# Optimization experiments

Measured on AMD Instinct MI355X. Metric: run time of the kernel, lower is better.

Reference implementation:

```python
import jax, jax.numpy as jnp
import numpy as np
import math

BS, L, DIM, H = 2, 1024, 1024, 16
DPH = DIM // H            # 64 dim per head
PHI_DIM = DPH * 1         # phi_size_ratio = 1
N_PROJS = 200
MIN_LOG_STD = math.log(1e-5)
SQRT_PHI = math.sqrt(PHI_DIM)


def setup_inputs() -> dict:
    key = jax.random.key(0)
    ks = jax.random.split(key, 8)
    lin = lambda k: jax.random.normal(k, (DIM, DIM), jnp.float32) * 0.02
    return {
        "x": jax.random.normal(ks[0], (BS, L, DIM), jnp.float32),
        "mask": jnp.ones((BS, L), dtype=jnp.bool_),
        "Wq": lin(ks[1]), "bq": jnp.zeros((DIM,), jnp.float32),
        "Wk": lin(ks[2]), "bk": jnp.zeros((DIM,), jnp.float32),
        "Wv": lin(ks[3]), "bv": jnp.zeros((DIM,), jnp.float32),
        "Wo": lin(ks[4]), "bo": jnp.zeros((DIM,), jnp.float32),
        "log_sigma": jnp.zeros((H, 1, DPH), jnp.float32),  # log(1.0) init
        "random_projs": jax.random.normal(ks[5], (N_PROJS, PHI_DIM, DPH), jnp.float32),
    }


def _phi(x, rp_scaled):
    # x: (b, l, h, d); rp_scaled: (h, phi, d). arccos features: relu(proj) / sqrt(phi_dim)
    x = x / jnp.maximum(jnp.linalg.norm(x, axis=-1, keepdims=True), 1e-12)
    px = jnp.einsum('blhd,hpd->blhp', x, rp_scaled)
    return jax.nn.relu(px) / SQRT_PHI


def _causal_rfa(phi_q, phi_k, v):
    # sequential S,z recurrence, time-major scan
    def step(carry, inp):
        S, z = carry
        pk, pq, vt = inp                       # (b,h,phi),(b,h,phi),(b,h,d)
        S = S + pk[..., :, None] * vt[..., None, :]
        z = z + pk
        num = jnp.einsum('bhp,bhpd->bhd', pq, S)
        den = jnp.einsum('bhp,bhp->bh', pq, z)
        return (S, z), num / jnp.maximum(den, 1e-5)[..., None]

    S0 = jnp.zeros((BS, H, PHI_DIM, DPH), jnp.float32)
    z0 = jnp.zeros((BS, H, PHI_DIM), jnp.float32)
    xs = (jnp.transpose(phi_k, (1, 0, 2, 3)),
          jnp.transpose(phi_q, (1, 0, 2, 3)),
          jnp.transpose(v, (1, 0, 2, 3)))
    _, h_t = jax.lax.scan(step, (S0, z0), xs)  # (l, b, h, d)
    return jnp.transpose(h_t, (1, 0, 2, 3))     # (b, l, h, d)


def reference(x, mask, Wq, bq, Wk, bk, Wv, bv, Wo, bo, log_sigma, random_projs):
    q = (x @ Wq.T + bq).reshape(BS, L, H, DPH)
    k = (x @ Wk.T + bk).reshape(BS, L, H, DPH)
    v = (x @ Wv.T + bv).reshape(BS, L, H, DPH)
    # eval mode: proj_id = 0 for every head
    scale = jnp.exp(jnp.maximum(log_sigma, MIN_LOG_STD))                  # (h,1,d)
    rp = scale * jnp.broadcast_to(random_projs[0], (H, PHI_DIM, DPH))     # (h,phi,d)
    phi_q = _phi(q, rp)
    phi_k = _phi(k, rp) * mask[:, :, None, None].astype(jnp.float32)
    h = _causal_rfa(phi_q, phi_k, v)                                      # (b,l,h,d)
    return h.reshape(BS, L, DIM) @ Wo.T + bo
```

## Files before the change

kernel.cpp:

```cpp
#include <hip/hip_runtime.h>


typedef unsigned short ushort_t;
typedef __attribute__((ext_vector_type(8))) __bf16 bf16x8;
typedef __attribute__((ext_vector_type(4))) float f32x4;

#define MLS -11.512925464970229f

__device__ __forceinline__ ushort_t f2b(float f) {
  union { float f; unsigned u; } v; v.f = f;
  unsigned r = v.u + 0x7FFFu + ((v.u >> 16) & 1u);
  return (ushort_t)(r >> 16);
}

__device__ __forceinline__ void gload16(const void* g, void* l) {
  __builtin_amdgcn_global_load_lds((__attribute__((address_space(1))) void*)(void*)g,
                                   (__attribute__((address_space(3))) void*)l, 16, 0, 0);
}

__device__ __forceinline__ f32x4 mfma_bf16(bf16x8 a, bf16x8 b, f32x4 c) {
  return __builtin_amdgcn_mfma_f32_16x16x32_bf16(a, b, c, 0, 0, 0);
}

__global__ __launch_bounds__(256) void convert_kernel(
    const float* __restrict__ x, const float* __restrict__ Wq, const float* __restrict__ Wk,
    const float* __restrict__ Wv, const float* __restrict__ Wo,
    const float* __restrict__ bq, const float* __restrict__ bk, const float* __restrict__ bv,
    const float* __restrict__ lsig, const float* __restrict__ rp0,
    ushort_t* __restrict__ xb, ushort_t* __restrict__ Wcat, ushort_t* __restrict__ Wob,
    float* __restrict__ bcat, float* __restrict__ sclbuf, ushort_t* __restrict__ rpb) {
  const size_t NX = (size_t)1 << 21, NW = (size_t)1 << 20;
  const size_t nch = (NX + 4 * NW) >> 3;
  size_t stride = (size_t)gridDim.x * 256;
  for (size_t i = (size_t)blockIdx.x * 256 + threadIdx.x; i < nch + 1024; i += stride) {
    if (i < nch) {
      size_t e = i << 3;
      const float* src; ushort_t* dst;
      if (e < NX)            { src = x  + e;               dst = xb   + e; }
      else if (e < NX + NW)  { src = Wq + (e - NX);        dst = Wcat + (e - NX); }
      else if (e < NX + 2*NW){ src = Wk + (e - NX - NW);   dst = Wcat + (e - NX); }
      else if (e < NX + 3*NW){ src = Wv + (e - NX - 2*NW); dst = Wcat + (e - NX); }
      else                   { src = Wo + (e - NX - 3*NW); dst = Wob  + (e - NX - 3*NW); }
      float4 a = *(const float4*)src, c = *(const float4*)(src + 4);
      uint4 u;
      u.x = (unsigned)f2b(a.x) | ((unsigned)f2b(a.y) << 16);
      u.y = (unsigned)f2b(a.z) | ((unsigned)f2b(a.w) << 16);
      u.z = (unsigned)f2b(c.x) | ((unsigned)f2b(c.y) << 16);
      u.w = (unsigned)f2b(c.z) | ((unsigned)f2b(c.w) << 16);
      *(uint4*)dst = u;
    } else {
      int j = (int)(i - nch);
      sclbuf[j] = expf(fmaxf(lsig[j], MLS));
      bcat[j] = bq[j]; bcat[1024 + j] = bk[j]; bcat[2048 + j] = bv[j];
#pragma unroll
      for (int jj = 0; jj < 4; ++jj) {
        int pe = j * 4 + jj;
        rpb[pe] = f2b(rp0[pe]);
      }
    }
  }
}

__global__ __launch_bounds__(256, 3) void qkvphi_kernel(
    const ushort_t* __restrict__ A, const ushort_t* __restrict__ Bm,
    const float* __restrict__ bias, const float* __restrict__ sclbuf,
    const ushort_t* __restrict__ rpb,
    ushort_t* __restrict__ phiq, ushort_t* __restrict__ phik, ushort_t* __restrict__ vbT) {
  __shared__ __align__(16) ushort_t smem[24576];
  const int K = 1024;
  int blk = blockIdx.x;
  int bx = blk % 48, by = blk / 48;
  int m0 = by << 7, n0 = bx << 6;
  int region = bx >> 4;
  int tid = threadIdx.x;
  int w = tid >> 6, l = tid & 63;
  int wm = w << 5;
  int lr = l & 15, lg = l >> 4;
  bf16x8 rpf[2][4];
  if (region < 2) {
#pragma unroll
    for (int kk = 0; kk < 2; ++kk)
#pragma unroll
      for (int ni = 0; ni < 4; ++ni)
        rpf[kk][ni] = *(const bf16x8*)(rpb + (ni*16 + lr)*64 + kk*32 + lg*8);
  }
  f32x4 acc[2][4] = {};
  auto stage = [&](int buf, int k0) {
    ushort_t* Ad = smem + buf*8192;
    ushort_t* Bd = smem + 16384 + buf*4096;
#pragma unroll
    for (int it = 0; it < 4; ++it) {
      int idx = it*256 + tid, row = idx >> 3, cg = idx & 7;
      gload16(A + (size_t)(m0 + row)*K + k0 + ((cg ^ (row & 7)) << 3), Ad + idx*8);
    }
#pragma unroll
    for (int it = 0; it < 2; ++it) {
      int idx = it*256 + tid, row = idx >> 3, cg = idx & 7;
      gload16(Bm + (size_t)(n0 + row)*K + k0 + ((cg ^ (row & 7)) << 3), Bd + idx*8);
    }
  };
  auto compute = [&](int buf) {
    const ushort_t* Ab = smem + buf*8192;
    const ushort_t* Bb = smem + 16384 + buf*4096;
#pragma unroll
    for (int kk = 0; kk < 2; ++kk) {
      bf16x8 af[2], bfr[4];
#pragma unroll
      for (int i = 0; i < 2; ++i) {
        int r = wm + i*16 + lr;
        af[i] = *(const bf16x8*)(Ab + r*64 + (((kk*4 + lg) ^ (r & 7)) << 3));
      }
#pragma unroll
      for (int i = 0; i < 4; ++i) {
        int r = i*16 + lr;
        bfr[i] = *(const bf16x8*)(Bb + r*64 + (((kk*4 + lg) ^ (r & 7)) << 3));
      }
#pragma unroll
      for (int mi = 0; mi < 2; ++mi)
#pragma unroll
        for (int ni = 0; ni < 4; ++ni)
          acc[mi][ni] = mfma_bf16(af[mi], bfr[ni], acc[mi][ni]);
    }
  };
  stage(0, 0);
  for (int t = 0; t < 15; ++t) {
    stage((t + 1) & 1, (t + 1) * 64);
    asm volatile("s_waitcnt vmcnt(6)" ::: "memory");
    __builtin_amdgcn_s_barrier();
    compute(t & 1);
    asm volatile("s_waitcnt lgkmcnt(0)" ::: "memory");
    __builtin_amdgcn_s_barrier();
  }
  asm volatile("s_waitcnt vmcnt(0)" ::: "memory");
  __builtin_amdgcn_s_barrier();
  compute(1);

  int b = m0 >> 10, tloc0 = m0 & 1023;
  float bias4[4];
#pragma unroll
  for (int ni = 0; ni < 4; ++ni) bias4[ni] = bias[n0 + ni*16 + lr];
  if (region == 2) {
    int dbase = n0 & 1023;
    int h = dbase >> 6;
    size_t hbase = ((size_t)(b*16 + h) << 16);
#pragma unroll
    for (int mi = 0; mi < 2; ++mi)
#pragma unroll
      for (int ni = 0; ni < 4; ++ni) {
        int d = (dbase + ni*16 + lr) & 63;
#pragma unroll
        for (int r = 0; r < 4; ++r) {
          int t = tloc0 + wm + mi*16 + lg*4 + r;
          int lloc = t & 127;
          int sv = (lloc & 7) | ((((lloc >> 3) ^ (d & 15)) & 15) << 3);
          vbT[hbase + (size_t)d*1024 + (t >> 7)*128 + sv] = f2b(acc[mi][ni][r] + bias4[ni]);
        }
      }
  } else {
    ushort_t* Ys = smem;
    int hglob = bx & 15;
    float scl4[4];
#pragma unroll
    for (int ni = 0; ni < 4; ++ni) scl4[ni] = sclbuf[hglob*64 + ni*16 + lr];
#pragma unroll
    for (int mi = 0; mi < 2; ++mi) {
      float v4[4][4];
      float ss[4] = {0.f, 0.f, 0.f, 0.f};
#pragma unroll
      for (int ni = 0; ni < 4; ++ni)
#pragma unroll
        for (int r = 0; r < 4; ++r) {
          float vv = acc[mi][ni][r] + bias4[ni];
          v4[ni][r] = vv;
          ss[r] += vv * vv;
        }
#pragma unroll
      for (int r = 0; r < 4; ++r) {
        float s = ss[r];
        s += __shfl_xor(s, 1); s += __shfl_xor(s, 2);
        s += __shfl_xor(s, 4); s += __shfl_xor(s, 8);
        ss[r] = 1.f / fmaxf(sqrtf(s), 1e-12f);
      }
#pragma unroll
      for (int ni = 0; ni < 4; ++ni) {
        int c = ni*16 + lr;
#pragma unroll
        for (int r = 0; r < 4; ++r) {
          int rl = wm + mi*16 + lg*4 + r;
          Ys[rl*64 + (((c >> 3) ^ (rl & 7)) << 3) + (c & 7)] = f2b(v4[ni][r] * ss[r] * scl4[ni]);
        }
      }
    }
    __syncthreads();
    ushort_t* dst = region ? phik : phiq;
    size_t obase = ((size_t)(b*16 + hglob) << 16);
    f32x4 acc2[2][4] = {};
#pragma unroll
    for (int kk = 0; kk < 2; ++kk) {
      bf16x8 af2[2];
#pragma unroll
      for (int mi = 0; mi < 2; ++mi) {
        int r = wm + mi*16 + lr;
        af2[mi] = *(const bf16x8*)(Ys + r*64 + (((kk*4 + lg) ^ (r & 7)) << 3));
      }
#pragma unroll
      for (int mi = 0; mi < 2; ++mi)
#pragma unroll
        for (int ni = 0; ni < 4; ++ni)
          acc2[mi][ni] = mfma_bf16(af2[mi], rpf[kk][ni], acc2[mi][ni]);
    }
#pragma unroll
    for (int mi = 0; mi < 2; ++mi)
#pragma unroll
      for (int ni = 0; ni < 4; ++ni)
#pragma unroll
        for (int r = 0; r < 4; ++r) {
          int t = tloc0 + wm + mi*16 + lg*4 + r;
          int p = ni*16 + lr;
          float val = fmaxf(acc2[mi][ni][r], 0.f) * 0.125f;
          int sp = (p & 7) | ((((p >> 3) ^ (t & 7)) & 7) << 3);
          dst[obase + (size_t)t*64 + sp] = f2b(val);
        }
  }
}

__global__ __launch_bounds__(256) void outproj_kernel(
    const ushort_t* __restrict__ A, const ushort_t* __restrict__ Bm,
    const float* __restrict__ bias, float* __restrict__ C) {
  __shared__ __align__(16) ushort_t smem[16384];
  const int K = 1024;
  int wid = (blockIdx.x & 7) * 64 + (blockIdx.x >> 3);
  int bx = wid & 15, by = wid >> 4;
  int m0 = by << 6, n0 = bx << 6;
  int tid = threadIdx.x, w = tid >> 6, l = tid & 63;
  int lr = l & 15, lg = l >> 4;
  auto stage = [&](int buf, int k0) {
    ushort_t* Ad = smem + buf*4096;
    ushort_t* Bd = smem + 8192 + buf*4096;
#pragma unroll
    for (int it = 0; it < 2; ++it) {
      int idx = it*256 + tid, row = idx >> 3, cg = idx & 7;
      gload16(A + (size_t)(m0 + row)*K + k0 + ((cg ^ (row & 7)) << 3), Ad + idx*8);
    }
#pragma unroll
    for (int it = 0; it < 2; ++it) {
      int idx = it*256 + tid, row = idx >> 3, cg = idx & 7;
      gload16(Bm + (size_t)(n0 + row)*K + k0 + ((cg ^ (row & 7)) << 3), Bd + idx*8);
    }
  };
  f32x4 acc[4] = {};
  auto compute = [&](int buf) {
    const ushort_t* Ab = smem + buf*4096;
    const ushort_t* Bb = smem + 8192 + buf*4096;
#pragma unroll
    for (int kk = 0; kk < 2; ++kk) {
      int ra = w*16 + lr;
      bf16x8 af = *(const bf16x8*)(Ab + ra*64 + (((kk*4 + lg) ^ (ra & 7)) << 3));
      bf16x8 bfr[4];
#pragma unroll
      for (int i = 0; i < 4; ++i) {
        int rb = i*16 + lr;
        bfr[i] = *(const bf16x8*)(Bb + rb*64 + (((kk*4 + lg) ^ (rb & 7)) << 3));
      }
#pragma unroll
      for (int ni = 0; ni < 4; ++ni)
        acc[ni] = mfma_bf16(af, bfr[ni], acc[ni]);
    }
  };
  stage(0, 0);
  for (int t = 0; t < 15; ++t) {
    stage((t + 1) & 1, (t + 1) * 64);
    asm volatile("s_waitcnt vmcnt(4)" ::: "memory");
    __builtin_amdgcn_s_barrier();
    compute(t & 1);
    asm volatile("s_waitcnt lgkmcnt(0)" ::: "memory");
    __builtin_amdgcn_s_barrier();
  }
  asm volatile("s_waitcnt vmcnt(0)" ::: "memory");
  __builtin_amdgcn_s_barrier();
  compute(1);
#pragma unroll
  for (int ni = 0; ni < 4; ++ni) {
    int col = n0 + ni*16 + lr;
    float bv = bias[col];
#pragma unroll
    for (int r = 0; r < 4; ++r)
      C[(size_t)(m0 + w*16 + lg*4 + r)*1024 + col] = acc[ni][r] + bv;
  }
}

__global__ __launch_bounds__(256) void attn_kernel(
    const ushort_t* __restrict__ phiq, const ushort_t* __restrict__ phik,
    const ushort_t* __restrict__ vbT, ushort_t* __restrict__ hb) {
  __shared__ __align__(16) ushort_t Qs[8192];
  __shared__ __align__(16) ushort_t Kd[2*8192];
  __shared__ __align__(16) ushort_t Vd[2*8192];
  __shared__ __align__(16) ushort_t Ps[16384];
  __shared__ float den_lds[128];
  int blk = blockIdx.x;
  int qt = blk >> 5, bh = blk & 31;
  int b = bh >> 4, h = bh & 15;
  int tid = threadIdx.x, w = tid >> 6, l = tid & 63;
  int lr = l & 15, lg = l >> 4;
  const ushort_t* pq = phiq + ((size_t)bh << 16) + qt*8192;
  const ushort_t* pk = phik + ((size_t)bh << 16);
  const ushort_t* pv = vbT  + ((size_t)bh << 16);
#pragma unroll
  for (int it = 0; it < 4; ++it) {
    int idx = it*256 + tid;
    gload16(pq + idx*8, Qs + idx*8);
  }
  auto stageKV = [&](int buf, int kt) {
#pragma unroll
    for (int it = 0; it < 4; ++it) {
      int idx = it*256 + tid;
      gload16(pk + kt*8192 + idx*8, Kd + buf*8192 + idx*8);
      gload16(pv + (idx >> 4)*1024 + kt*128 + (idx & 15)*8, Vd + buf*8192 + idx*8);
    }
  };
  f32x4 nacc[2][4] = {};
  float den[2] = {0.f, 0.f};
  auto tile = [&](int buf, bool diag) {
    const ushort_t* Ks = Kd + buf*8192;
    const ushort_t* Vs = Vd + buf*8192;
    bf16x8 qf[2][2];
#pragma unroll
    for (int qi = 0; qi < 2; ++qi)
#pragma unroll
      for (int ks = 0; ks < 2; ++ks) {
        int q = w*32 + qi*16 + lr;
        qf[qi][ks] = *(const bf16x8*)(Qs + q*64 + (((ks*4 + lg) ^ (q & 7)) << 3));
      }
    f32x4 sfr[8][2] = {};
#pragma unroll
    for (int kf = 0; kf < 8; ++kf) {
#pragma unroll
      for (int ks = 0; ks < 2; ++ks) {
        int kloc = kf*16 + lr;
        bf16x8 af = *(const bf16x8*)(Ks + kloc*64 + (((ks*4 + lg) ^ (kloc & 7)) << 3));
        sfr[kf][0] = mfma_bf16(af, qf[0][ks], sfr[kf][0]);
        sfr[kf][1] = mfma_bf16(af, qf[1][ks], sfr[kf][1]);
      }
    }
#pragma unroll
    for (int kf = 0; kf < 8; ++kf) {
#pragma unroll
      for (int qi = 0; qi < 2; ++qi) {
        int q = w*32 + qi*16 + lr;
        f32x4 v4 = sfr[kf][qi];
        if (diag) {
          int keyb = kf*16 + lg*4;
#pragma unroll
          for (int r = 0; r < 4; ++r)
            if (keyb + r > q) v4[r] = 0.f;
        }
        den[qi] += v4[0] + v4[1] + v4[2] + v4[3];
        unsigned long long u = (unsigned long long)f2b(v4[0])
                             | ((unsigned long long)f2b(v4[1]) << 16)
                             | ((unsigned long long)f2b(v4[2]) << 32)
                             | ((unsigned long long)f2b(v4[3]) << 48);
        int chunk = (2*kf + (lg >> 1)) ^ (q & 7);
        *(unsigned long long*)(Ps + q*128 + chunk*8 + (lg & 1)*4) = u;
      }
    }
#pragma unroll
    for (int ks = 0; ks < 4; ++ks) {
      bf16x8 pa[2];
#pragma unroll
      for (int qi = 0; qi < 2; ++qi) {
        int q = w*32 + qi*16 + lr;
        pa[qi] = *(const bf16x8*)(Ps + q*128 + (((4*ks + lg) ^ (q & 7)) << 3));
      }
#pragma unroll
      for (int df = 0; df < 4; ++df) {
        int d = df*16 + lr;
        bf16x8 vf = *(const bf16x8*)(Vs + d*128 + (((4*ks + lg) ^ (d & 15)) << 3));
        nacc[0][df] = mfma_bf16(pa[0], vf, nacc[0][df]);
        nacc[1][df] = mfma_bf16(pa[1], vf, nacc[1][df]);
      }
    }
  };
  stageKV(0, 0);
  for (int kt = 0; kt < qt; ++kt) {
    stageKV((kt + 1) & 1, kt + 1);
    asm volatile("s_waitcnt vmcnt(8)" ::: "memory");
    __builtin_amdgcn_s_barrier();
    tile(kt & 1, false);
    asm volatile("s_waitcnt lgkmcnt(0)" ::: "memory");
    __builtin_amdgcn_s_barrier();
  }
  asm volatile("s_waitcnt vmcnt(0)" ::: "memory");
  __builtin_amdgcn_s_barrier();
  tile(qt & 1, true);
  den[0] += __shfl_xor(den[0], 16); den[0] += __shfl_xor(den[0], 32);
  den[1] += __shfl_xor(den[1], 16); den[1] += __shfl_xor(den[1], 32);
  if (lg == 0) {
    den_lds[w*32 + lr]      = den[0];
    den_lds[w*32 + 16 + lr] = den[1];
  }
  __syncthreads();
#pragma unroll
  for (int qi = 0; qi < 2; ++qi)
#pragma unroll
    for (int df = 0; df < 4; ++df)
#pragma unroll
      for (int r = 0; r < 4; ++r) {
        int qloc = w*32 + qi*16 + lg*4 + r;
        int d = df*16 + lr;
        float dd = fmaxf(den_lds[qloc], 1e-5f);
        float val = nacc[qi][df][r] / dd;
        hb[((size_t)(b*1024 + qt*128 + qloc))*1024 + h*64 + d] = f2b(val);
      }
}

extern "C" void kernel_launch(void* const* d_in, const int* in_sizes, int n_in,
                              void* d_out, int out_size, void* d_ws, size_t ws_size,
                              hipStream_t stream) {
  const float* x  = (const float*)d_in[0];
  const float* Wq = (const float*)d_in[2];
  const float* bq = (const float*)d_in[3];
  const float* Wk = (const float*)d_in[4];
  const float* bk = (const float*)d_in[5];
  const float* Wv = (const float*)d_in[6];
  const float* bv = (const float*)d_in[7];
  const float* Wo = (const float*)d_in[8];
  const float* bo = (const float*)d_in[9];
  const float* ls = (const float*)d_in[10];
  const float* rp = (const float*)d_in[11];

  char* ws = (char*)d_ws;
  size_t off = 0;
  auto alloc = [&](size_t bytes) { char* p = ws + off; off += (bytes + 255) & ~(size_t)255; return p; };
  ushort_t* xb     = (ushort_t*)alloc((size_t)2048*1024*2);
  ushort_t* Wcat   = (ushort_t*)alloc((size_t)3072*1024*2);
  ushort_t* Wob    = (ushort_t*)alloc((size_t)1024*1024*2);
  float*    bcat   = (float*)   alloc((size_t)3072*4);
  float*    sclbuf = (float*)   alloc((size_t)1024*4);
  ushort_t* rpb    = (ushort_t*)alloc((size_t)64*64*2);
  ushort_t* phiq   = (ushort_t*)alloc((size_t)32*1024*64*2);
  ushort_t* phik   = (ushort_t*)alloc((size_t)32*1024*64*2);
  ushort_t* vbT    = (ushort_t*)alloc((size_t)32*64*1024*2);
  ushort_t* hb     = (ushort_t*)alloc((size_t)2048*1024*2);

  convert_kernel<<<1024, 256, 0, stream>>>(x, Wq, Wk, Wv, Wo, bq, bk, bv, ls, rp,
                                           xb, Wcat, Wob, bcat, sclbuf, rpb);
  qkvphi_kernel<<<768, 256, 0, stream>>>(xb, Wcat, bcat, sclbuf, rpb, phiq, phik, vbT);
  attn_kernel<<<256, 256, 0, stream>>>(phiq, phik, vbT, hb);
  outproj_kernel<<<512, 256, 0, stream>>>(hb, Wob, bo, (float*)d_out);
}
```

Baseline: 62.17 us.

## Compute Q, K and V for one head per block with 512-thread tiles

Restructures the QKV+phi GEMM so each block covers a 128-row tile across all of Q, K and V for a single head (192 output columns), using 8 waves instead of 4. Waves split into Q/K halves that each also take half of the V columns, and each wave normalizes and projects its own 32x64 slice through a private LDS region. The A tile is now loaded once for all three projections, which cuts redundant x traffic. In exchange the grid shrinks from 768 blocks to 256, and each block uses more LDS and registers, which may lower occupancy on a GPU with many CUs.

```diff
diff --git a/kernel.cpp b/kernel.cpp
--- a/kernel.cpp
+++ b/kernel.cpp
@@ -61,71 +61,70 @@
   }
 }
 
-__global__ __launch_bounds__(256, 3) void qkvphi_kernel(
+__global__ __launch_bounds__(512, 2) void qkvphi_kernel(
     const ushort_t* __restrict__ A, const ushort_t* __restrict__ Bm,
     const float* __restrict__ bias, const float* __restrict__ sclbuf,
     const ushort_t* __restrict__ rpb,
     ushort_t* __restrict__ phiq, ushort_t* __restrict__ phik, ushort_t* __restrict__ vbT) {
-  __shared__ __align__(16) ushort_t smem[24576];
+  __shared__ __align__(16) ushort_t smem[40960];
   const int K = 1024;
   int blk = blockIdx.x;
-  int bx = blk % 48, by = blk / 48;
-  int m0 = by << 7, n0 = bx << 6;
-  int region = bx >> 4;
+  int hg = blk & 15, by = blk >> 4;
+  int m0 = by << 7;
   int tid = threadIdx.x;
   int w = tid >> 6, l = tid & 63;
-  int wm = w << 5;
+  int wr = w & 3, wc = w >> 2;
   int lr = l & 15, lg = l >> 4;
   bf16x8 rpf[2][4];
-  if (region < 2) {
-#pragma unroll
-    for (int kk = 0; kk < 2; ++kk)
-#pragma unroll
-      for (int ni = 0; ni < 4; ++ni)
-        rpf[kk][ni] = *(const bf16x8*)(rpb + (ni*16 + lr)*64 + kk*32 + lg*8);
-  }
-  f32x4 acc[2][4] = {};
+#pragma unroll
+  for (int kk = 0; kk < 2; ++kk)
+#pragma unroll
+    for (int ni = 0; ni < 4; ++ni)
+      rpf[kk][ni] = *(const bf16x8*)(rpb + (ni*16 + lr)*64 + kk*32 + lg*8);
+
+  f32x4 acc[2][6] = {};
   auto stage = [&](int buf, int k0) {
     ushort_t* Ad = smem + buf*8192;
-    ushort_t* Bd = smem + 16384 + buf*4096;
-#pragma unroll
-    for (int it = 0; it < 4; ++it) {
-      int idx = it*256 + tid, row = idx >> 3, cg = idx & 7;
+    ushort_t* Bd = smem + 16384 + buf*12288;
+#pragma unroll
+    for (int it = 0; it < 2; ++it) {
+      int idx = it*512 + tid, row = idx >> 3, cg = idx & 7;
       gload16(A + (size_t)(m0 + row)*K + k0 + ((cg ^ (row & 7)) << 3), Ad + idx*8);
     }
 #pragma unroll
-    for (int it = 0; it < 2; ++it) {
-      int idx = it*256 + tid, row = idx >> 3, cg = idx & 7;
-      gload16(Bm + (size_t)(n0 + row)*K + k0 + ((cg ^ (row & 7)) << 3), Bd + idx*8);
+    for (int it = 0; it < 3; ++it) {
+      int idx = it*512 + tid, row = idx >> 3, cg = idx & 7;
+      int grow = (row >> 6)*1024 + hg*64 + (row & 63);
+      gload16(Bm + (size_t)grow*K + k0 + ((cg ^ (row & 7)) << 3), Bd + idx*8);
     }
   };
   auto compute = [&](int buf) {
     const ushort_t* Ab = smem + buf*8192;
-    const ushort_t* Bb = smem + 16384 + buf*4096;
+    const ushort_t* Bb = smem + 16384 + buf*12288;
 #pragma unroll
     for (int kk = 0; kk < 2; ++kk) {
-      bf16x8 af[2], bfr[4];
+      bf16x8 af[2], bfr[6];
 #pragma unroll
       for (int i = 0; i < 2; ++i) {
-        int r = wm + i*16 + lr;
+        int r = wr*32 + i*16 + lr;
         af[i] = *(const bf16x8*)(Ab + r*64 + (((kk*4 + lg) ^ (r & 7)) << 3));
       }
 #pragma unroll
-      for (int i = 0; i < 4; ++i) {
-        int r = i*16 + lr;
-        bfr[i] = *(const bf16x8*)(Bb + r*64 + (((kk*4 + lg) ^ (r & 7)) << 3));
+      for (int i = 0; i < 6; ++i) {
+        int brow = (i < 4) ? (wc*64 + i*16 + lr) : (128 + wc*32 + (i - 4)*16 + lr);
+        bfr[i] = *(const bf16x8*)(Bb + brow*64 + (((kk*4 + lg) ^ (brow & 7)) << 3));
       }
 #pragma unroll
       for (int mi = 0; mi < 2; ++mi)
 #pragma unroll
-        for (int ni = 0; ni < 4; ++ni)
+        for (int ni = 0; ni < 6; ++ni)
           acc[mi][ni] = mfma_bf16(af[mi], bfr[ni], acc[mi][ni]);
     }
   };
   stage(0, 0);
   for (int t = 0; t < 15; ++t) {
     stage((t + 1) & 1, (t + 1) * 64);
-    asm volatile("s_waitcnt vmcnt(6)" ::: "memory");
+    asm volatile("s_waitcnt vmcnt(5)" ::: "memory");
     __builtin_amdgcn_s_barrier();
     compute(t & 1);
     asm volatile("s_waitcnt lgkmcnt(0)" ::: "memory");
@@ -134,34 +133,36 @@
   asm volatile("s_waitcnt vmcnt(0)" ::: "memory");
   __builtin_amdgcn_s_barrier();
   compute(1);
+  __syncthreads();
 
   int b = m0 >> 10, tloc0 = m0 & 1023;
-  float bias4[4];
-#pragma unroll
-  for (int ni = 0; ni < 4; ++ni) bias4[ni] = bias[n0 + ni*16 + lr];
-  if (region == 2) {
-    int dbase = n0 & 1023;
-    int h = dbase >> 6;
-    size_t hbase = ((size_t)(b*16 + h) << 16);
+  {
+    size_t hbase = ((size_t)(b*16 + hg) << 16);
+    float bv2[2];
+#pragma unroll
+    for (int j = 0; j < 2; ++j) bv2[j] = bias[2048 + hg*64 + wc*32 + j*16 + lr];
 #pragma unroll
     for (int mi = 0; mi < 2; ++mi)
 #pragma unroll
-      for (int ni = 0; ni < 4; ++ni) {
-        int d = (dbase + ni*16 + lr) & 63;
+      for (int j = 0; j < 2; ++j) {
+        int d = wc*32 + j*16 + lr;
 #pragma unroll
         for (int r = 0; r < 4; ++r) {
-          int t = tloc0 + wm + mi*16 + lg*4 + r;
+          int t = tloc0 + wr*32 + mi*16 + lg*4 + r;
           int lloc = t & 127;
           int sv = (lloc & 7) | ((((lloc >> 3) ^ (d & 15)) & 15) << 3);
-          vbT[hbase + (size_t)d*1024 + (t >> 7)*128 + sv] = f2b(acc[mi][ni][r] + bias4[ni]);
+          vbT[hbase + (size_t)d*1024 + (t >> 7)*128 + sv] = f2b(acc[mi][4 + j][r] + bv2[j]);
         }
       }
-  } else {
-    ushort_t* Ys = smem;
-    int hglob = bx & 15;
-    float scl4[4];
-#pragma unroll
-    for (int ni = 0; ni < 4; ++ni) scl4[ni] = sclbuf[hglob*64 + ni*16 + lr];
+  }
+  ushort_t* Ys = smem + w*2048;
+  {
+    float bias4[4], scl4[4];
+#pragma unroll
+    for (int ni = 0; ni < 4; ++ni) {
+      bias4[ni] = bias[wc*1024 + hg*64 + ni*16 + lr];
+      scl4[ni]  = sclbuf[hg*64 + ni*16 + lr];
+    }
 #pragma unroll
     for (int mi = 0; mi < 2; ++mi) {
       float v4[4][4];
@@ -186,22 +187,23 @@
         int c = ni*16 + lr;
 #pragma unroll
         for (int r = 0; r < 4; ++r) {
-          int rl = wm + mi*16 + lg*4 + r;
+          int rl = mi*16 + lg*4 + r;
           Ys[rl*64 + (((c >> 3) ^ (rl & 7)) << 3) + (c & 7)] = f2b(v4[ni][r] * ss[r] * scl4[ni]);
         }
       }
     }
-    __syncthreads();
-    ushort_t* dst = region ? phik : phiq;
-    size_t obase = ((size_t)(b*16 + hglob) << 16);
+  }
+  {
+    ushort_t* dst = wc ? phik : phiq;
+    size_t obase = ((size_t)(b*16 + hg) << 16);
     f32x4 acc2[2][4] = {};
 #pragma unroll
     for (int kk = 0; kk < 2; ++kk) {
       bf16x8 af2[2];
 #pragma unroll
       for (int mi = 0; mi < 2; ++mi) {
-        int r = wm + mi*16 + lr;
-        af2[mi] = *(const bf16x8*)(Ys + r*64 + (((kk*4 + lg) ^ (r & 7)) << 3));
+        int rl = mi*16 + lr;
+        af2[mi] = *(const bf16x8*)(Ys + rl*64 + (((kk*4 + lg) ^ (rl & 7)) << 3));
       }
 #pragma unroll
       for (int mi = 0; mi < 2; ++mi)
@@ -215,7 +217,7 @@
       for (int ni = 0; ni < 4; ++ni)
 #pragma unroll
         for (int r = 0; r < 4; ++r) {
-          int t = tloc0 + wm + mi*16 + lg*4 + r;
+          int t = tloc0 + wr*32 + mi*16 + lg*4 + r;
           int p = ni*16 + lr;
           float val = fmaxf(acc2[mi][ni][r], 0.f) * 0.125f;
           int sp = (p & 7) | ((((p >> 3) ^ (t & 7)) & 7) << 3);
@@ -444,7 +446,7 @@
 
   convert_kernel<<<1024, 256, 0, stream>>>(x, Wq, Wk, Wv, Wo, bq, bk, bv, ls, rp,
                                            xb, Wcat, Wob, bcat, sclbuf, rpb);
-  qkvphi_kernel<<<768, 256, 0, stream>>>(xb, Wcat, bcat, sclbuf, rpb, phiq, phik, vbT);
+  qkvphi_kernel<<<256, 512, 0, stream>>>(xb, Wcat, bcat, sclbuf, rpb, phiq, phik, vbT);
   attn_kernel<<<256, 256, 0, stream>>>(phiq, phik, vbT, hb);
   outproj_kernel<<<512, 256, 0, stream>>>(hb, Wob, bo, (float*)d_out);
 }
```

After: 62.00 us. About the same (-0.3%).
